# Kernel tuning notes

Hardware: AMD Instinct MI355X
Metric: run time of the kernel (lower is better)

## Reference

```python
import jax, jax.numpy as jnp
import numpy as np

NEG_SLOPE = 0.2

def gatv2_conv(x, src, dst, Wl, Wr, att, b, num_nodes):
    # GATv2: e = att . leaky_relu(Wl x_src + Wr x_dst); segment softmax over dst; scatter-add of alpha * Wl x_src
    xl = x @ Wl  # [N, out]
    xr = x @ Wr  # [N, out]
    m = xl[src] + xr[dst]                        # [E, out] edge gather
    e = jax.nn.leaky_relu(m, NEG_SLOPE) @ att    # [E]
    emax = jax.ops.segment_max(e, dst, num_segments=num_nodes)
    ee = jnp.exp(e - emax[dst])
    denom = jax.ops.segment_sum(ee, dst, num_segments=num_nodes)
    alpha = ee / denom[dst]                      # [E]
    out = jax.ops.segment_sum(alpha[:, None] * xl[src], dst, num_segments=num_nodes)
    return out + b

def setup_inputs() -> dict:
    key = jax.random.key(0)
    ks = jax.random.split(key, 24)
    N, E, F, H, B = 40000, 640000, 128, 128, 64
    inp = {
        'x': jax.random.normal(ks[0], (N, F), dtype=jnp.float32),
        'edge_index': jax.random.randint(ks[1], (2, E), 0, N),
        'batch': jnp.sort(jax.random.randint(ks[2], (N,), 0, B)),
        'day': jax.random.randint(ks[3], (B,), 0, 7),
        'hour': jax.random.randint(ks[4], (B,), 0, 24),
    }
    def glorot(k, shape):
        lim = float(np.sqrt(6.0 / (shape[0] + shape[1])))
        return jax.random.uniform(k, shape, jnp.float32, -lim, lim)
    # GATv2 layers (heads=1)
    inp['Wl1'] = glorot(ks[5], (F, H)); inp['Wr1'] = glorot(ks[6], (F, H))
    inp['att1'] = glorot(ks[7], (H, 1))[:, 0]; inp['b1'] = jnp.zeros((H,), jnp.float32)
    inp['Wl2'] = glorot(ks[8], (H, H)); inp['Wr2'] = glorot(ks[9], (H, H))
    inp['att2'] = glorot(ks[10], (H, 1))[:, 0]; inp['b2'] = jnp.zeros((H,), jnp.float32)
    inp['Wl3'] = glorot(ks[11], (H, H)); inp['Wr3'] = glorot(ks[12], (H, H))
    inp['att3'] = glorot(ks[13], (H, 1))[:, 0]; inp['b3'] = jnp.zeros((H,), jnp.float32)
    # embeddings
    inp['day_tab'] = jax.random.normal(ks[14], (7, 64), dtype=jnp.float32)
    inp['hour_tab'] = jax.random.normal(ks[15], (24, 64), dtype=jnp.float32)
    # MLP head (weights stored [in, out])
    inp['W1'] = glorot(ks[16], (256, 256)); inp['bl1'] = jnp.zeros((256,), jnp.float32)
    inp['W2'] = glorot(ks[17], (256, 256)); inp['bl2'] = jnp.zeros((256,), jnp.float32)
    inp['W3'] = glorot(ks[18], (256, 1));   inp['bl3'] = jnp.zeros((1,), jnp.float32)
    return inp

def reference(x, edge_index, batch, day, hour,
              Wl1, Wr1, att1, b1, Wl2, Wr2, att2, b2, Wl3, Wr3, att3, b3,
              day_tab, hour_tab, W1, bl1, W2, bl2, W3, bl3):
    N = x.shape[0]
    B = day.shape[0]
    # add self loops (PyG default add_self_loops=True)
    loops = jnp.arange(N)
    src = jnp.concatenate([edge_index[0], loops])
    dst = jnp.concatenate([edge_index[1], loops])
    h = gatv2_conv(x, src, dst, Wl1, Wr1, att1, b1, N)
    h = jax.nn.relu(h)
    h = gatv2_conv(h, src, dst, Wl2, Wr2, att2, b2, N)
    h = jax.nn.relu(h)
    h = gatv2_conv(h, src, dst, Wl3, Wr3, att3, b3, N)
    # global mean pool over graphs
    sums = jax.ops.segment_sum(h, batch, num_segments=B)
    cnts = jax.ops.segment_sum(jnp.ones((N,), h.dtype), batch, num_segments=B)
    pooled = sums / jnp.maximum(cnts, 1.0)[:, None]      # [B, 128]
    feats = jnp.concatenate([pooled, day_tab[day], hour_tab[hour]], axis=1)  # [B, 256]
    z = jax.nn.relu(feats @ W1 + bl1)
    z = jax.nn.relu(z @ W2 + bl2)
    return z @ W3 + bl3  # [B, 1]
```

## Files before the change

### kernel.cpp

```cpp
#include <hip/hip_runtime.h>
#include <math.h>

#define NEG_SLOPE 0.2f
#define POOL_CHUNKS 8
#define SOFF 8.0f

typedef __attribute__((ext_vector_type(8))) short bf16x8;
typedef __attribute__((ext_vector_type(4))) float f32x4;

__device__ __forceinline__ void split_bf16(float x, short& hi, short& lo) {
    unsigned u = __float_as_uint(x);
    unsigned uh = u & 0xFFFF0000u;
    float r = x - __uint_as_float(uh);
    hi = (short)(uh >> 16);
    lo = (short)(__float_as_uint(r) >> 16);
}

__device__ __forceinline__ unsigned f2bf_rne(float x) {
    unsigned u = __float_as_uint(x);
    return (u + 0x7fffu + ((u >> 16) & 1u)) >> 16;
}

__global__ __launch_bounds__(256, 1) void node_gemm(
    const float* __restrict__ h, const float* __restrict__ Wl,
    const float* __restrict__ Wr, unsigned* __restrict__ xlb,
    float* __restrict__ xr, int N, int nTiles)
{
    const int w   = threadIdx.x >> 6;
    const int l   = threadIdx.x & 63;
    const int l15 = l & 15, lg = l >> 4;

    const float* __restrict__ Wsel = (w < 2) ? Wl : Wr;
    const int cbase = (w & 1) * 64;

    bf16x8 bh[4][4];
    #pragma unroll
    for (int ct = 0; ct < 4; ++ct) {
        const int c = cbase + ct * 16 + l15;
        #pragma unroll
        for (int kt = 0; kt < 4; ++kt) {
            #pragma unroll
            for (int i = 0; i < 8; ++i) {
                float v = Wsel[(kt * 32 + lg * 8 + i) * 128 + c];
                bh[ct][kt][i] = (short)f2bf_rne(v);
            }
        }
    }

    for (int tile = blockIdx.x; tile < nTiles; tile += gridDim.x) {
        const int row0 = tile * 64;

        f32x4 acc[4][4];
        #pragma unroll
        for (int rt = 0; rt < 4; ++rt)
            #pragma unroll
            for (int ct = 0; ct < 4; ++ct)
                acc[rt][ct] = (f32x4){0.f, 0.f, 0.f, 0.f};

        #pragma unroll
        for (int rt = 0; rt < 4; ++rt) {
            int row = row0 + rt * 16 + l15;
            int rowc = row < N ? row : N - 1;
            bf16x8 ah[4], al[4];
            #pragma unroll
            for (int kt = 0; kt < 4; ++kt) {
                const float4 v0 = *(const float4*)&h[(size_t)rowc * 128 + kt * 32 + lg * 8];
                const float4 v1 = *(const float4*)&h[(size_t)rowc * 128 + kt * 32 + lg * 8 + 4];
                const float vv[8] = {v0.x, v0.y, v0.z, v0.w, v1.x, v1.y, v1.z, v1.w};
                #pragma unroll
                for (int i = 0; i < 8; ++i) {
                    short hi, lo; split_bf16(vv[i], hi, lo);
                    ah[kt][i] = hi; al[kt][i] = lo;
                }
            }
            #pragma unroll
            for (int kt = 0; kt < 4; ++kt) {
                #pragma unroll
                for (int ct = 0; ct < 4; ++ct) {
                    acc[rt][ct] = __builtin_amdgcn_mfma_f32_16x16x32_bf16(
                        ah[kt], bh[ct][kt], acc[rt][ct], 0, 0, 0);
                    acc[rt][ct] = __builtin_amdgcn_mfma_f32_16x16x32_bf16(
                        al[kt], bh[ct][kt], acc[rt][ct], 0, 0, 0);
                }
            }
        }

        if (w < 2) {
            #pragma unroll
            for (int rt = 0; rt < 4; ++rt) {
                #pragma unroll
                for (int ct = 0; ct < 4; ++ct) {
                    #pragma unroll
                    for (int j = 0; j < 4; ++j) {
                        int row = row0 + rt * 16 + lg * 4 + j;
                        unsigned o = f2bf_rne(acc[rt][ct][j]);
                        unsigned pr = (unsigned)__shfl_xor((int)o, 1);
                        if (!(l15 & 1) && row < N) {
                            int cp = (cbase + ct * 16 + l15) >> 1;
                            xlb[(size_t)row * 64 + cp] = o | (pr << 16);
                        }
                    }
                }
            }
        } else {
            #pragma unroll
            for (int rt = 0; rt < 4; ++rt) {
                #pragma unroll
                for (int ct = 0; ct < 4; ++ct) {
                    #pragma unroll
                    for (int j = 0; j < 4; ++j) {
                        int row = row0 + rt * 16 + lg * 4 + j;
                        if (row < N)
                            xr[(size_t)row * 128 + cbase + ct * 16 + l15] = acc[rt][ct][j];
                    }
                }
            }
        }
    }
}

__global__ __launch_bounds__(256) void zero_ints(int* __restrict__ p, int n)
{
    int i = blockIdx.x * blockDim.x + threadIdx.x;
    if (i < n) p[i] = 0;
}

__global__ __launch_bounds__(256) void edge_hist(
    const int* __restrict__ ei, int* __restrict__ deg, int E)
{
    int eid = blockIdx.x * blockDim.x + threadIdx.x;
    if (eid >= E) return;
    atomicAdd(&deg[ei[E + eid]], 1);
}

__global__ __launch_bounds__(256) void scan_block(
    const int* __restrict__ in, int* __restrict__ out_excl,
    int* __restrict__ bsum, int N)
{
    __shared__ int sm[256];
    int t = threadIdx.x, i = blockIdx.x * 256 + t;
    int v = (i < N) ? in[i] : 0;
    sm[t] = v;
    __syncthreads();
    int x = v;
    for (int o = 1; o < 256; o <<= 1) {
        int u = (t >= o) ? sm[t - o] : 0;
        __syncthreads();
        x += u; sm[t] = x;
        __syncthreads();
    }
    if (i < N) out_excl[i] = x - v;
    if (t == 255) bsum[blockIdx.x] = x;
}

__global__ __launch_bounds__(256) void scan_sums(int* __restrict__ bsum, int nb)
{
    __shared__ int sm[256];
    int t = threadIdx.x;
    int v = (t < nb) ? bsum[t] : 0;
    sm[t] = v;
    __syncthreads();
    int x = v;
    for (int o = 1; o < 256; o <<= 1) {
        int u = (t >= o) ? sm[t - o] : 0;
        __syncthreads();
        x += u; sm[t] = x;
        __syncthreads();
    }
    if (t < nb) bsum[t] = x - v;
}

__global__ __launch_bounds__(256) void scan_final(
    const int* __restrict__ excl, const int* __restrict__ bsum,
    int* __restrict__ rowptr, int* __restrict__ cursor, int N, int E)
{
    int i = blockIdx.x * blockDim.x + threadIdx.x;
    if (i > N) return;
    int v = (i < N) ? (excl[i] + bsum[i >> 8]) : E;
    rowptr[i] = v;
    if (i < N) cursor[i] = v;
}

__global__ __launch_bounds__(256) void edge_fill(
    const int* __restrict__ ei, int* __restrict__ cursor,
    unsigned short* __restrict__ srcs, int E)
{
    int eid = blockIdx.x * blockDim.x + threadIdx.x;
    if (eid >= E) return;
    int src = ei[eid], dst = ei[E + eid];
    int pos = atomicAdd(&cursor[dst], 1);
    srcs[pos] = (unsigned short)src;
}

__global__ __launch_bounds__(256) void gatv2_aggregate(
    const unsigned* __restrict__ xlb, const float* __restrict__ xr,
    const int* __restrict__ rowptr, const unsigned short* __restrict__ srcs,
    const float* __restrict__ att, const float* __restrict__ b,
    float* __restrict__ hout, int N, int do_relu)
{
    int n = blockIdx.x * 4 + (threadIdx.x >> 6);
    if (n >= N) return;
    const int lane = threadIdx.x & 63;
    const int hl = lane & 15;
    const int g  = lane >> 4;

    float xr8[8], at8[8];
    {
        const float4 a0 = *(const float4*)&xr[(size_t)n * 128 + hl * 8];
        const float4 a1 = *(const float4*)&xr[(size_t)n * 128 + hl * 8 + 4];
        xr8[0]=a0.x; xr8[1]=a0.y; xr8[2]=a0.z; xr8[3]=a0.w;
        xr8[4]=a1.x; xr8[5]=a1.y; xr8[6]=a1.z; xr8[7]=a1.w;
        const float4 t0 = *(const float4*)&att[hl * 8];
        const float4 t1 = *(const float4*)&att[hl * 8 + 4];
        at8[0]=t0.x; at8[1]=t0.y; at8[2]=t0.z; at8[3]=t0.w;
        at8[4]=t1.x; at8[5]=t1.y; at8[6]=t1.z; at8[7]=t1.w;
    }

    int r0 = rowptr[n], r1 = rowptr[n + 1];
    float s = 0.f;
    float acc[8];
    #pragma unroll
    for (int c = 0; c < 8; ++c) acc[c] = 0.f;

    auto unpack = [&](const uint4 q, float* vv) {
        unsigned u;
        u = q.x; vv[0] = __uint_as_float(u << 16); vv[1] = __uint_as_float(u & 0xFFFF0000u);
        u = q.y; vv[2] = __uint_as_float(u << 16); vv[3] = __uint_as_float(u & 0xFFFF0000u);
        u = q.z; vv[4] = __uint_as_float(u << 16); vv[5] = __uint_as_float(u & 0xFFFF0000u);
        u = q.w; vv[6] = __uint_as_float(u << 16); vv[7] = __uint_as_float(u & 0xFFFF0000u);
    };
    auto score = [&](const float* vv) -> float {
        float p = 0.f;
        #pragma unroll
        for (int c = 0; c < 8; ++c) {
            float t = vv[c] + xr8[c];
            t = fmaxf(t, NEG_SLOPE * t);
            p += t * at8[c];
        }
        return p;
    };
    auto online = [&](float p, const float* vv) {
        float w = __expf(p - SOFF);
        s += w;
        #pragma unroll
        for (int c = 0; c < 8; ++c) acc[c] += w * vv[c];
    };

    if (g == 0) {
        const uint4 qs = *(const uint4*)&xlb[(size_t)n * 64 + hl * 4];
        float vs[8];
        unpack(qs, vs);
        float ps = score(vs);
        #pragma unroll
        for (int off = 1; off < 16; off <<= 1) ps += __shfl_xor(ps, off);
        online(ps, vs);
    }

    int j = r0 + g;
    int sa = (j < r1) ? (int)srcs[j] : 0;
    int sb = (j + 4 < r1) ? (int)srcs[j + 4] : sa;
    for (; j + 4 < r1; j += 8) {
        const uint4 qa = *(const uint4*)&xlb[(size_t)sa * 64 + hl * 4];
        const uint4 qb = *(const uint4*)&xlb[(size_t)sb * 64 + hl * 4];
        int jn0 = (j + 8  < r1) ? j + 8  : j;
        int jn1 = (j + 12 < r1) ? j + 12 : j;
        int sna = (int)srcs[jn0], snb = (int)srcs[jn1];
        float va[8], vb[8];
        unpack(qa, va); unpack(qb, vb);
        float pa = score(va), pb = score(vb);
        #pragma unroll
        for (int off = 1; off < 16; off <<= 1) {
            pa += __shfl_xor(pa, off);
            pb += __shfl_xor(pb, off);
        }
        online(pa, va);
        online(pb, vb);
        sa = sna; sb = snb;
    }
    if (j < r1) {
        const uint4 qa = *(const uint4*)&xlb[(size_t)sa * 64 + hl * 4];
        float va[8];
        unpack(qa, va);
        float pa = score(va);
        #pragma unroll
        for (int off = 1; off < 16; off <<= 1) pa += __shfl_xor(pa, off);
        online(pa, va);
    }

    s += __shfl_xor(s, 16); s += __shfl_xor(s, 32);
    #pragma unroll
    for (int c = 0; c < 8; ++c) {
        acc[c] += __shfl_xor(acc[c], 16);
        acc[c] += __shfl_xor(acc[c], 32);
    }

    if (g == 0) {
        float inv = 1.f / s;
        float o[8];
        #pragma unroll
        for (int c = 0; c < 8; ++c) {
            o[c] = acc[c] * inv + b[hl * 8 + c];
            if (do_relu) o[c] = fmaxf(o[c], 0.f);
        }
        *(float4*)&hout[(size_t)n * 128 + hl * 8]     = make_float4(o[0], o[1], o[2], o[3]);
        *(float4*)&hout[(size_t)n * 128 + hl * 8 + 4] = make_float4(o[4], o[5], o[6], o[7]);
    }
}

__global__ __launch_bounds__(256) void graph_bounds(
    const int* __restrict__ batch, int* __restrict__ gstart, int N, int B)
{
    int b = blockIdx.x * blockDim.x + threadIdx.x;
    if (b > B) return;
    int lo = 0, hi = N;
    while (lo < hi) {
        int mid = (lo + hi) >> 1;
        if (batch[mid] < b) lo = mid + 1; else hi = mid;
    }
    gstart[b] = lo;
}

__global__ __launch_bounds__(256) void pool_graph(
    const float* __restrict__ h, const int* __restrict__ gstart,
    float* __restrict__ pooled)
{
    __shared__ float sm[128];
    const int b = blockIdx.x / POOL_CHUNKS;
    const int chunk = blockIdx.x % POOL_CHUNKS;
    const int t = threadIdx.x;
    const int col = t & 127, hf = t >> 7;
    const int r0 = gstart[b], r1 = gstart[b + 1];
    const int len = r1 - r0;
    const int c0 = r0 + (int)(((long long)len * chunk) / POOL_CHUNKS);
    const int c1 = r0 + (int)(((long long)len * (chunk + 1)) / POOL_CHUNKS);
    float s = 0.f;
    for (int r = c0 + hf; r < c1; r += 2)
        s += h[(size_t)r * 128 + col];
    if (hf) sm[col] = s;
    __syncthreads();
    if (!hf) pooled[(size_t)(b * POOL_CHUNKS + chunk) * 128 + col] = s + sm[col];
}

__global__ __launch_bounds__(256) void mlp_head(
    const float* __restrict__ pooled, const int* __restrict__ gstart,
    const int* __restrict__ day, const int* __restrict__ hour,
    const float* __restrict__ day_tab, const float* __restrict__ hour_tab,
    const float* __restrict__ W1, const float* __restrict__ bl1,
    const float* __restrict__ W2, const float* __restrict__ bl2,
    const float* __restrict__ W3, const float* __restrict__ bl3,
    float* __restrict__ out)
{
    __shared__ float f0[256], f1[256];
    const int b = blockIdx.x, t = threadIdx.x;
    float c = fmaxf((float)(gstart[b + 1] - gstart[b]), 1.f);
    if (t < 128) {
        float sum = 0.f;
        #pragma unroll
        for (int ch = 0; ch < POOL_CHUNKS; ++ch)
            sum += pooled[(size_t)(b * POOL_CHUNKS + ch) * 128 + t];
        f0[t] = sum / c;
    }
    else if (t < 192) f0[t] = day_tab[day[b] * 64 + (t - 128)];
    else              f0[t] = hour_tab[hour[b] * 64 + (t - 192)];
    __syncthreads();
    float a = bl1[t];
    for (int k = 0; k < 256; ++k) a += f0[k] * W1[k * 256 + t];
    f1[t] = a > 0.f ? a : 0.f;
    __syncthreads();
    a = bl2[t];
    for (int k = 0; k < 256; ++k) a += f1[k] * W2[k * 256 + t];
    __syncthreads();
    f0[t] = a > 0.f ? a : 0.f;
    __syncthreads();
    f1[t] = f0[t] * W3[t];
    __syncthreads();
    for (int s2 = 128; s2 > 0; s2 >>= 1) {
        if (t < s2) f1[t] += f1[t + s2];
        __syncthreads();
    }
    if (t == 0) out[b] = f1[0] + bl3[0];
}

extern "C" void kernel_launch(void* const* d_in, const int* in_sizes, int n_in,
                              void* d_out, int out_size, void* d_ws, size_t ws_size,
                              hipStream_t stream) {
    const float* x        = (const float*)d_in[0];
    const int*   ei       = (const int*)d_in[1];
    const int*   batch    = (const int*)d_in[2];
    const int*   day      = (const int*)d_in[3];
    const int*   hour     = (const int*)d_in[4];
    const float* Wl[3]  = { (const float*)d_in[5],  (const float*)d_in[9],  (const float*)d_in[13] };
    const float* Wr[3]  = { (const float*)d_in[6],  (const float*)d_in[10], (const float*)d_in[14] };
    const float* att[3] = { (const float*)d_in[7],  (const float*)d_in[11], (const float*)d_in[15] };
    const float* bb[3]  = { (const float*)d_in[8],  (const float*)d_in[12], (const float*)d_in[16] };
    const float* day_tab  = (const float*)d_in[17];
    const float* hour_tab = (const float*)d_in[18];
    const float* W1 = (const float*)d_in[19]; const float* bl1 = (const float*)d_in[20];
    const float* W2 = (const float*)d_in[21]; const float* bl2 = (const float*)d_in[22];
    const float* W3 = (const float*)d_in[23]; const float* bl3 = (const float*)d_in[24];
    float* out = (float*)d_out;

    const int N  = in_sizes[0] / 128;
    const int E  = in_sizes[1] / 2;
    const int B  = in_sizes[3];

    char* ws = (char*)d_ws;
    size_t off = 0;
    auto alloc = [&](size_t bytes) -> void* {
        void* p = ws + off;
        off += (bytes + 255) & ~(size_t)255;
        return p;
    };
    const size_t NB = (size_t)N * 128 * sizeof(float);
    unsigned* xlb = (unsigned*)alloc((size_t)N * 64 * sizeof(unsigned));
    float* xr     = (float*)alloc(NB);
    float* hbuf   = (float*)alloc(NB);
    int*   deg    = (int*)alloc((size_t)N * sizeof(int));
    int*   excl   = (int*)alloc((size_t)N * sizeof(int));
    int*   bsum   = (int*)alloc(256 * sizeof(int));
    int*   rowptr = (int*)alloc((size_t)(N + 1) * sizeof(int));
    int*   cursor = (int*)alloc((size_t)N * sizeof(int));
    unsigned short* srcs = (unsigned short*)alloc((size_t)E * sizeof(unsigned short));
    int*   gstart = (int*)alloc((size_t)(B + 1) * sizeof(int));
    float* pooled = (float*)alloc((size_t)B * POOL_CHUNKS * 128 * sizeof(float));
    (void)ws_size;

    const int nb = (N + 255) / 256;
    const int edge_grid  = (E + 255) / 256;
    const int node_grid4 = (N + 3) / 4;
    const int nTiles     = (N + 63) / 64;

    zero_ints<<<nb, 256, 0, stream>>>(deg, N);
    edge_hist<<<edge_grid, 256, 0, stream>>>(ei, deg, E);
    scan_block<<<nb, 256, 0, stream>>>(deg, excl, bsum, N);
    scan_sums<<<1, 256, 0, stream>>>(bsum, nb);
    scan_final<<<(N + 256) / 256, 256, 0, stream>>>(excl, bsum, rowptr, cursor, N, E);
    edge_fill<<<edge_grid, 256, 0, stream>>>(ei, cursor, srcs, E);

    const float* hin = x;
    for (int l = 0; l < 3; ++l) {
        node_gemm<<<nTiles, 256, 0, stream>>>(hin, Wl[l], Wr[l], xlb, xr, N, nTiles);
        gatv2_aggregate<<<node_grid4, 256, 0, stream>>>(
            xlb, xr, rowptr, srcs, att[l], bb[l], hbuf, N, l < 2 ? 1 : 0);
        hin = hbuf;
    }

    graph_bounds<<<1, 256, 0, stream>>>(batch, gstart, N, B);
    pool_graph<<<B * POOL_CHUNKS, 256, 0, stream>>>(hbuf, gstart, pooled);
    mlp_head<<<B, 256, 0, stream>>>(pooled, gstart, day, hour, day_tab, hour_tab,
                                    W1, bl1, W2, bl2, W3, bl3, out);
}
```

Measured before the change: 289.9 us.

## Store layer activations as bf16 and drop hi/lo split MFMA in node GEMM

Converts the input features to packed bf16 in a new pre-pass. Each aggregate kernel now writes its output as packed bf16 instead of fp32, so the next node GEMM reads half the bytes and issues one MFMA per tile step instead of the hi+lo pair. Pooling is adapted to read packed bf16. This roughly halves activation traffic and GEMM math, at the cost of dropping the split-precision compensation, so activations carry bf16 rounding error through all three layers.

```diff
diff --git a/kernel.cpp b/kernel.cpp
--- a/kernel.cpp
+++ b/kernel.cpp
@@ -8,21 +8,22 @@
 typedef __attribute__((ext_vector_type(8))) short bf16x8;
 typedef __attribute__((ext_vector_type(4))) float f32x4;
 
-__device__ __forceinline__ void split_bf16(float x, short& hi, short& lo) {
-    unsigned u = __float_as_uint(x);
-    unsigned uh = u & 0xFFFF0000u;
-    float r = x - __uint_as_float(uh);
-    hi = (short)(uh >> 16);
-    lo = (short)(__float_as_uint(r) >> 16);
-}
-
 __device__ __forceinline__ unsigned f2bf_rne(float x) {
     unsigned u = __float_as_uint(x);
     return (u + 0x7fffu + ((u >> 16) & 1u)) >> 16;
 }
 
+__global__ __launch_bounds__(256) void pack_bf16(
+    const float* __restrict__ x, unsigned* __restrict__ xpk, int n)
+{
+    int i = blockIdx.x * blockDim.x + threadIdx.x;
+    if (i >= n) return;
+    const float2 v = *(const float2*)&x[(size_t)i * 2];
+    xpk[i] = f2bf_rne(v.x) | (f2bf_rne(v.y) << 16);
+}
+
 __global__ __launch_bounds__(256, 1) void node_gemm(
-    const float* __restrict__ h, const float* __restrict__ Wl,
+    const unsigned* __restrict__ hpk, const float* __restrict__ Wl,
     const float* __restrict__ Wr, unsigned* __restrict__ xlb,
     float* __restrict__ xr, int N, int nTiles)
 {
@@ -61,26 +62,16 @@
         for (int rt = 0; rt < 4; ++rt) {
             int row = row0 + rt * 16 + l15;
             int rowc = row < N ? row : N - 1;
-            bf16x8 ah[4], al[4];
-            #pragma unroll
-            for (int kt = 0; kt < 4; ++kt) {
-                const float4 v0 = *(const float4*)&h[(size_t)rowc * 128 + kt * 32 + lg * 8];
-                const float4 v1 = *(const float4*)&h[(size_t)rowc * 128 + kt * 32 + lg * 8 + 4];
-                const float vv[8] = {v0.x, v0.y, v0.z, v0.w, v1.x, v1.y, v1.z, v1.w};
-                #pragma unroll
-                for (int i = 0; i < 8; ++i) {
-                    short hi, lo; split_bf16(vv[i], hi, lo);
-                    ah[kt][i] = hi; al[kt][i] = lo;
-                }
-            }
+            bf16x8 ah[4];
+            #pragma unroll
+            for (int kt = 0; kt < 4; ++kt)
+                ah[kt] = *(const bf16x8*)&hpk[(size_t)rowc * 64 + kt * 16 + lg * 4];
             #pragma unroll
             for (int kt = 0; kt < 4; ++kt) {
                 #pragma unroll
                 for (int ct = 0; ct < 4; ++ct) {
                     acc[rt][ct] = __builtin_amdgcn_mfma_f32_16x16x32_bf16(
                         ah[kt], bh[ct][kt], acc[rt][ct], 0, 0, 0);
-                    acc[rt][ct] = __builtin_amdgcn_mfma_f32_16x16x32_bf16(
-                        al[kt], bh[ct][kt], acc[rt][ct], 0, 0, 0);
                 }
             }
         }
@@ -196,7 +187,7 @@
     const unsigned* __restrict__ xlb, const float* __restrict__ xr,
     const int* __restrict__ rowptr, const unsigned short* __restrict__ srcs,
     const float* __restrict__ att, const float* __restrict__ b,
-    float* __restrict__ hout, int N, int do_relu)
+    unsigned* __restrict__ hout, int N, int do_relu)
 {
     int n = blockIdx.x * 4 + (threadIdx.x >> 6);
     if (n >= N) return;
@@ -296,14 +287,15 @@
 
     if (g == 0) {
         float inv = 1.f / s;
-        float o[8];
-        #pragma unroll
-        for (int c = 0; c < 8; ++c) {
-            o[c] = acc[c] * inv + b[hl * 8 + c];
-            if (do_relu) o[c] = fmaxf(o[c], 0.f);
-        }
-        *(float4*)&hout[(size_t)n * 128 + hl * 8]     = make_float4(o[0], o[1], o[2], o[3]);
-        *(float4*)&hout[(size_t)n * 128 + hl * 8 + 4] = make_float4(o[4], o[5], o[6], o[7]);
+        unsigned pk[4];
+        #pragma unroll
+        for (int c = 0; c < 4; ++c) {
+            float o0 = acc[2 * c]     * inv + b[hl * 8 + 2 * c];
+            float o1 = acc[2 * c + 1] * inv + b[hl * 8 + 2 * c + 1];
+            if (do_relu) { o0 = fmaxf(o0, 0.f); o1 = fmaxf(o1, 0.f); }
+            pk[c] = f2bf_rne(o0) | (f2bf_rne(o1) << 16);
+        }
+        *(uint4*)&hout[(size_t)n * 64 + hl * 4] = make_uint4(pk[0], pk[1], pk[2], pk[3]);
     }
 }
 
@@ -321,24 +313,34 @@
 }
 
 __global__ __launch_bounds__(256) void pool_graph(
-    const float* __restrict__ h, const int* __restrict__ gstart,
+    const unsigned* __restrict__ h, const int* __restrict__ gstart,
     float* __restrict__ pooled)
 {
-    __shared__ float sm[128];
+    __shared__ float sm0[4][64];
+    __shared__ float sm1[4][64];
     const int b = blockIdx.x / POOL_CHUNKS;
     const int chunk = blockIdx.x % POOL_CHUNKS;
     const int t = threadIdx.x;
-    const int col = t & 127, hf = t >> 7;
+    const int colp = t & 63, part = t >> 6;
     const int r0 = gstart[b], r1 = gstart[b + 1];
     const int len = r1 - r0;
     const int c0 = r0 + (int)(((long long)len * chunk) / POOL_CHUNKS);
     const int c1 = r0 + (int)(((long long)len * (chunk + 1)) / POOL_CHUNKS);
-    float s = 0.f;
-    for (int r = c0 + hf; r < c1; r += 2)
-        s += h[(size_t)r * 128 + col];
-    if (hf) sm[col] = s;
-    __syncthreads();
-    if (!hf) pooled[(size_t)(b * POOL_CHUNKS + chunk) * 128 + col] = s + sm[col];
+    float s0 = 0.f, s1 = 0.f;
+    for (int r = c0 + part; r < c1; r += 4) {
+        unsigned u = h[(size_t)r * 64 + colp];
+        s0 += __uint_as_float(u << 16);
+        s1 += __uint_as_float(u & 0xFFFF0000u);
+    }
+    sm0[part][colp] = s0;
+    sm1[part][colp] = s1;
+    __syncthreads();
+    if (part == 0) {
+        #pragma unroll
+        for (int p = 1; p < 4; ++p) { s0 += sm0[p][colp]; s1 += sm1[p][colp]; }
+        float* dst = &pooled[(size_t)(b * POOL_CHUNKS + chunk) * 128 + colp * 2];
+        dst[0] = s0; dst[1] = s1;
+    }
 }
 
 __global__ __launch_bounds__(256) void mlp_head(
@@ -411,10 +413,11 @@
         off += (bytes + 255) & ~(size_t)255;
         return p;
     };
-    const size_t NB = (size_t)N * 128 * sizeof(float);
-    unsigned* xlb = (unsigned*)alloc((size_t)N * 64 * sizeof(unsigned));
-    float* xr     = (float*)alloc(NB);
-    float* hbuf   = (float*)alloc(NB);
+    const size_t NPK = (size_t)N * 64 * sizeof(unsigned);
+    unsigned* xpk  = (unsigned*)alloc(NPK);
+    unsigned* xlb  = (unsigned*)alloc(NPK);
+    float*    xr   = (float*)alloc((size_t)N * 128 * sizeof(float));
+    unsigned* hbuf = (unsigned*)alloc(NPK);
     int*   deg    = (int*)alloc((size_t)N * sizeof(int));
     int*   excl   = (int*)alloc((size_t)N * sizeof(int));
     int*   bsum   = (int*)alloc(256 * sizeof(int));
@@ -437,7 +440,9 @@
     scan_final<<<(N + 256) / 256, 256, 0, stream>>>(excl, bsum, rowptr, cursor, N, E);
     edge_fill<<<edge_grid, 256, 0, stream>>>(ei, cursor, srcs, E);
 
-    const float* hin = x;
+    pack_bf16<<<(N * 64 + 255) / 256, 256, 0, stream>>>(x, xpk, N * 64);
+
+    const unsigned* hin = xpk;
     for (int l = 0; l < 3; ++l) {
         node_gemm<<<nTiles, 256, 0, stream>>>(hin, Wl[l], Wr[l], xlb, xr, N, nTiles);
         gatv2_aggregate<<<node_grid4, 256, 0, stream>>>(
```

Result: faster. 274.7 us (-5.3%).
